# Kernel tuning notes

Measured on AMD Instinct MI355X. Metric: run time of the kernel, lower is better.

The kernel has to match this reference:

```python
import jax, jax.numpy as jnp
import numpy as np

B, SQ, SK, D, H = 8, 1024, 1024, 1024, 16
DH = D // H  # attention head size = 64
LN_EPS = 1e-5


def _layer_norm(x, g, b):
    m = jnp.mean(x, axis=-1, keepdims=True)
    v = jnp.mean(jnp.square(x - m), axis=-1, keepdims=True)
    return (x - m) * jax.lax.rsqrt(v + LN_EPS) * g + b


def setup_inputs() -> dict:
    key = jax.random.key(0)
    ks = jax.random.split(key, 12)
    s = 0.02
    return {
        "hidden_states": jax.random.normal(ks[0], (B, SQ, D), jnp.float32),
        "context": jax.random.normal(ks[1], (B, SK, D), jnp.float32),
        "Wq": jax.random.normal(ks[2], (D, D), jnp.float32) * s,
        "bq": jnp.zeros((D,), jnp.float32),
        "Wk": jax.random.normal(ks[3], (D, D), jnp.float32) * s,
        "bk": jnp.zeros((D,), jnp.float32),
        "Wv": jax.random.normal(ks[4], (D, D), jnp.float32) * s,
        "bv": jnp.zeros((D,), jnp.float32),
        "Wobs": jax.random.normal(ks[5], (D, D), jnp.float32) * s,
        "bobs": jnp.zeros((D,), jnp.float32),
        "Wmat": jax.random.normal(ks[6], (D, D), jnp.float32) * s,
        "bmat": jnp.zeros((D,), jnp.float32),
        "ln_g": jnp.ones((D,), jnp.float32),
        "ln_b": jnp.zeros((D,), jnp.float32),
    }


def reference(hidden_states, context, Wq, bq, Wk, bk, Wv, bv,
              Wobs, bobs, Wmat, bmat, ln_g, ln_b):
    # QKV projections (torch Linear: x @ W.T + b)
    q = hidden_states @ Wq.T + bq            # [B, SQ, D]
    k = context @ Wk.T + bk                  # [B, SK, D]
    v = context @ Wv.T + bv                  # [B, SK, D]

    # ---- Guide_Block: single-head SDPA over full D, then linear->ReLU->LN ----
    # (dropout is identity in eval mode)
    score = jnp.einsum('bqd,bkd->bqk', q, k) / np.sqrt(D)   # [B, SQ, SK]
    attn = jax.nn.softmax(score, axis=-1)
    gctx = jnp.einsum('bqk,bkd->bqd', attn, v)              # [B, SQ, D]
    new_q = _layer_norm(jax.nn.relu(gctx @ Wobs.T + bobs), ln_g, ln_b)
    new_k = _layer_norm(jax.nn.relu(k @ Wmat.T + bmat), ln_g, ln_b)

    # ---- Multi-head attention with guided q/k and original v ----
    qh = new_q.reshape(B, SQ, H, DH).transpose(0, 2, 1, 3)  # [B, H, SQ, DH]
    kh = new_k.reshape(B, SK, H, DH).transpose(0, 2, 1, 3)
    vh = v.reshape(B, SK, H, DH).transpose(0, 2, 1, 3)
    scores = jnp.einsum('bhqd,bhkd->bhqk', qh, kh) / np.sqrt(DH)
    probs = jax.nn.softmax(scores, axis=-1)                 # attn dropout = identity (eval)
    out = jnp.einsum('bhqk,bhkd->bhqd', probs, vh)          # [B, H, SQ, DH]
    return out.transpose(0, 2, 1, 3).reshape(B, SQ, D)
```

## Files before the change

kernel.cpp:

```cpp
#include <hip/hip_runtime.h>
#include <hip/hip_bf16.h>

#define DEV __device__ __forceinline__

using bf16x8 = __attribute__((ext_vector_type(8))) short;
using f32x4  = __attribute__((ext_vector_type(4))) float;
using f32x16 = __attribute__((ext_vector_type(16))) float;

#define MFMA16(a, b, c) __builtin_amdgcn_mfma_f32_16x16x32_bf16((a), (b), (c), 0, 0, 0)
#define MFMA32(a, b, c) __builtin_amdgcn_mfma_f32_32x32x16_bf16((a), (b), (c), 0, 0, 0)

#define GLOAD_LDS16(gp, lp)                                                        \
  __builtin_amdgcn_global_load_lds(                                               \
      (__attribute__((address_space(1))) unsigned int*)(gp),                      \
      (__attribute__((address_space(3))) unsigned int*)(lp), 16, 0, 0)

DEV float b2f(unsigned short u) {
  union { float f; unsigned u; } x; x.u = ((unsigned)u) << 16; return x.f;
}
DEV unsigned short f2b(float f) {
  union { float f; unsigned u; } x; x.f = f;
  unsigned r = x.u + 0x7FFFu + ((x.u >> 16) & 1u);
  return (unsigned short)(r >> 16);
}
DEV float fexp2(float x) {
  float r;
  asm("v_exp_f32 %0, %1" : "=v"(r) : "v"(x));
  return r;
}

__global__ __launch_bounds__(256) void detect_kernel(
    const unsigned short* __restrict__ hs, int* __restrict__ flag) {
  __shared__ int red[4];
  const int t = threadIdx.x;
  const ushort4* p = (const ushort4*)hs;
  int cnt = 0;
#pragma unroll
  for (int j = 0; j < 16; j++) {
    ushort4 u = p[j * 256 + t];
    cnt += (((u.x >> 7) & 0xFF) == 0xFF) + (((u.y >> 7) & 0xFF) == 0xFF) +
           (((u.z >> 7) & 0xFF) == 0xFF) + (((u.w >> 7) & 0xFF) == 0xFF);
  }
#pragma unroll
  for (int off = 32; off >= 1; off >>= 1) cnt += __shfl_xor(cnt, off, 64);
  if ((t & 63) == 0) red[t >> 6] = cnt;
  __syncthreads();
  if (t == 0) flag[0] = (red[0] + red[1] + red[2] + red[3] >= 4) ? 1 : 0;
}

__global__ __launch_bounds__(256) void convert2_kernel(
    const void* __restrict__ s0, const void* __restrict__ s1,
    unsigned short* __restrict__ d0, unsigned short* __restrict__ d1,
    const int* __restrict__ flag) {
  const int bid = blockIdx.x;
  const void* src;
  unsigned short* dst;
  long off;
  if (bid < 8192) { src = s0; dst = d0; off = (long)bid * 1024; }
  else            { src = s1; dst = d1; off = (long)(bid - 8192) * 1024; }
  const long i = off + threadIdx.x * 4;
  ushort4 o;
  if (*flag) {
    float4 f = ((const float4*)src)[i >> 2];
    o.x = f2b(f.x); o.y = f2b(f.y); o.z = f2b(f.z); o.w = f2b(f.w);
  } else {
    o = ((const ushort4*)src)[i >> 2];
  }
  ((ushort4*)dst)[i >> 2] = o;
}

__global__ __launch_bounds__(256) void convert_w_kernel(
    const void* __restrict__ s0, const void* __restrict__ s1,
    const void* __restrict__ s2, const void* __restrict__ s3,
    const void* __restrict__ s4, unsigned short* __restrict__ dst,
    const int* __restrict__ flag) {
  const void* srcs[5] = {s0, s1, s2, s3, s4};
  const void* src = srcs[blockIdx.y];
  unsigned short* d = dst + (long)blockIdx.y * 1048576;
  const int i = (blockIdx.x * 256 + threadIdx.x) * 4;
  ushort4 o;
  if (*flag) {
    float4 f = ((const float4*)src)[i >> 2];
    o.x = f2b(f.x); o.y = f2b(f.y); o.z = f2b(f.z); o.w = f2b(f.w);
  } else {
    o = ((const ushort4*)src)[i >> 2];
  }
  ((ushort4*)d)[i >> 2] = o;
}

__global__ __launch_bounds__(256) void convert_vec_kernel(
    const void* __restrict__ s0, const void* __restrict__ s1,
    const void* __restrict__ s2, const void* __restrict__ s3,
    const void* __restrict__ s4, const void* __restrict__ s5,
    const void* __restrict__ s6, unsigned short* __restrict__ dst,
    const int* __restrict__ flag) {
  const void* srcs[7] = {s0, s1, s2, s3, s4, s5, s6};
  const void* src = srcs[blockIdx.x];
  unsigned short* d = dst + blockIdx.x * 1024;
  const int i = threadIdx.x * 4;
  ushort4 o;
  if (*flag) {
    float4 f = ((const float4*)src)[i >> 2];
    o.x = f2b(f.x); o.y = f2b(f.y); o.z = f2b(f.z); o.w = f2b(f.w);
  } else {
    o = ((const ushort4*)src)[i >> 2];
  }
  ((ushort4*)d)[i >> 2] = o;
}

template <int RELU, int OUTBF16, int BIAS, int SPLIT>
__global__ __launch_bounds__(256, 4) void gemm_bt_kernel(
    const unsigned short* __restrict__ A, const unsigned short* __restrict__ B,
    const unsigned short* __restrict__ bias, void* __restrict__ Cv,
    void* __restrict__ Cv2, int M, int N, int K, long sA_, long sB_, long sC_,
    float scale) {
  __shared__ unsigned short sA[2][128 * 32];
  __shared__ unsigned short sB[2][128 * 32];
  const int t = threadIdx.x;
  const int wave = t >> 6, lane = t & 63;
  const int quad = lane >> 4, col = lane & 15;
  const int wm = wave >> 1, wn = wave & 1;
  const long zb = blockIdx.z;
  const unsigned short* Ab = A + zb * sA_ + (long)blockIdx.x * 128 * K;
  const unsigned short* Bb = B + zb * sB_ + (long)blockIdx.y * 128 * K;
  const int r0 = t >> 2;
  const int c0 = (t & 3) * 8;

  f32x4 zz = {0.f, 0.f, 0.f, 0.f};
  f32x4 acc[4][4];
#pragma unroll
  for (int i = 0; i < 4; i++)
#pragma unroll
    for (int j = 0; j < 4; j++) acc[i][j] = zz;

  for (int k0 = 0; k0 < K; k0 += 64) {
    __syncthreads();
#pragma unroll
    for (int p = 0; p < 2; p++) {
      GLOAD_LDS16(Ab + (long)r0 * K + k0 + p * 32 + c0,        &sA[p][t * 8]);
      GLOAD_LDS16(Ab + (long)(64 + r0) * K + k0 + p * 32 + c0, &sA[p][2048 + t * 8]);
      GLOAD_LDS16(Bb + (long)r0 * K + k0 + p * 32 + c0,        &sB[p][t * 8]);
      GLOAD_LDS16(Bb + (long)(64 + r0) * K + k0 + p * 32 + c0, &sB[p][2048 + t * 8]);
    }
    __syncthreads();
#pragma unroll
    for (int p = 0; p < 2; p++) {
      bf16x8 af[4], bfr[4];
#pragma unroll
      for (int mi = 0; mi < 4; mi++)
        af[mi] = *(const bf16x8*)&sA[p][(wm * 64 + mi * 16 + col) * 32 + quad * 8];
#pragma unroll
      for (int ni = 0; ni < 4; ni++)
        bfr[ni] = *(const bf16x8*)&sB[p][(wn * 64 + ni * 16 + col) * 32 + quad * 8];
#pragma unroll
      for (int mi = 0; mi < 4; mi++)
#pragma unroll
        for (int ni = 0; ni < 4; ni++)
          acc[mi][ni] = MFMA16(af[mi], bfr[ni], acc[mi][ni]);
    }
  }

  const int Rm = blockIdx.x * 128 + wm * 64;
  const int Cn = blockIdx.y * 128 + wn * 64;
  float bs[4];
#pragma unroll
  for (int ni = 0; ni < 4; ni++)
    bs[ni] = BIAS ? b2f(bias[Cn + ni * 16 + col]) : 0.f;

  unsigned short* Cb = (unsigned short*)Cv;
  int Nw = N, cadj = 0;
  if (SPLIT) {
    Nw = N >> 1;
    if (blockIdx.y >= (gridDim.y >> 1)) { Cb = (unsigned short*)Cv2; cadj = Nw; }
  }
#pragma unroll
  for (int mi = 0; mi < 4; mi++)
#pragma unroll
    for (int ni = 0; ni < 4; ni++)
#pragma unroll
      for (int r = 0; r < 4; r++) {
        int rr = Rm + mi * 16 + quad * 4 + r;
        int cc = Cn + ni * 16 + col;
        float v = acc[mi][ni][r] * scale + bs[ni];
        if (RELU) v = fmaxf(v, 0.f);
        if (OUTBF16)
          Cb[zb * sC_ + (long)rr * Nw + (cc - cadj)] = f2b(v);
        else
          ((float*)Cv)[zb * sC_ + (long)rr * N + cc] = v;
      }
}

__global__ __launch_bounds__(256) void softmax_kernel(
    const float* __restrict__ S, unsigned short* __restrict__ P) {
  __shared__ float red[8];
  const long row = blockIdx.x;
  const int t = threadIdx.x;
  const float4 v4 = ((const float4*)(S + row * 1024))[t];
  float x[4] = {v4.x, v4.y, v4.z, v4.w};
  float m = fmaxf(fmaxf(x[0], x[1]), fmaxf(x[2], x[3]));
#pragma unroll
  for (int off = 32; off >= 1; off >>= 1) m = fmaxf(m, __shfl_xor(m, off, 64));
  if ((t & 63) == 0) red[t >> 6] = m;
  __syncthreads();
  m = fmaxf(fmaxf(red[0], red[1]), fmaxf(red[2], red[3]));
  float e[4], s = 0.f;
#pragma unroll
  for (int i = 0; i < 4; i++) { e[i] = __expf(x[i] - m); s += e[i]; }
#pragma unroll
  for (int off = 32; off >= 1; off >>= 1) s += __shfl_xor(s, off, 64);
  __syncthreads();
  if ((t & 63) == 0) red[4 + (t >> 6)] = s;
  __syncthreads();
  s = red[4] + red[5] + red[6] + red[7];
  float inv = 1.f / s;
  ushort4 o;
  o.x = f2b(e[0] * inv); o.y = f2b(e[1] * inv);
  o.z = f2b(e[2] * inv); o.w = f2b(e[3] * inv);
  ((ushort4*)(P + row * 1024))[t] = o;
}

DEV float block_sum(float v, float* red, int t) {
#pragma unroll
  for (int off = 32; off >= 1; off >>= 1) v += __shfl_xor(v, off, 64);
  __syncthreads();
  if ((t & 63) == 0) red[t >> 6] = v;
  __syncthreads();
  return red[0] + red[1] + red[2] + red[3];
}

__global__ __launch_bounds__(256) void layernorm2_kernel(
    const unsigned short* __restrict__ X0, const unsigned short* __restrict__ X1,
    const unsigned short* __restrict__ G, const unsigned short* __restrict__ Bt,
    unsigned short* __restrict__ Y0, unsigned short* __restrict__ Y1) {
  __shared__ float red[4];
  const int bid = blockIdx.x;
  const unsigned short* X;
  unsigned short* Y;
  if (bid < 8192) { X = X0 + (long)bid * 1024; Y = Y0 + (long)bid * 1024; }
  else { X = X1 + (long)(bid - 8192) * 1024; Y = Y1 + (long)(bid - 8192) * 1024; }
  const int t = threadIdx.x;
  ushort4 u = ((const ushort4*)X)[t];
  float x[4] = {b2f(u.x), b2f(u.y), b2f(u.z), b2f(u.w)};
  float s = x[0] + x[1] + x[2] + x[3];
  float mean = block_sum(s, red, t) * (1.f / 1024.f);
  float d0 = x[0] - mean, d1 = x[1] - mean, d2 = x[2] - mean, d3 = x[3] - mean;
  float vs = d0 * d0 + d1 * d1 + d2 * d2 + d3 * d3;
  float var = block_sum(vs, red, t) * (1.f / 1024.f);
  float rs = rsqrtf(var + 1e-5f);
  ushort4 gu = ((const ushort4*)G)[t];
  ushort4 bu = ((const ushort4*)Bt)[t];
  ushort4 o;
  o.x = f2b(d0 * rs * b2f(gu.x) + b2f(bu.x));
  o.y = f2b(d1 * rs * b2f(gu.y) + b2f(bu.y));
  o.z = f2b(d2 * rs * b2f(gu.z) + b2f(bu.z));
  o.w = f2b(d3 * rs * b2f(gu.w) + b2f(bu.w));
  ((ushort4*)Y)[t] = o;
}

__global__ __launch_bounds__(256) void transpose_kernel(
    const unsigned short* __restrict__ V, unsigned short* __restrict__ VT) {
  __shared__ unsigned short tile[32][33];
  const int b = blockIdx.z;
  const int d0 = blockIdx.x * 32, sk0 = blockIdx.y * 32;
  const int tx = threadIdx.x & 31, ty = threadIdx.x >> 5;
#pragma unroll
  for (int i = 0; i < 32; i += 8)
    tile[ty + i][tx] = V[((long)(b * 1024 + sk0 + ty + i)) * 1024 + d0 + tx];
  __syncthreads();
#pragma unroll
  for (int i = 0; i < 32; i += 8)
    VT[((long)(b * 1024 + d0 + ty + i)) * 1024 + sk0 + tx] = tile[tx][ty + i];
}

__global__ __launch_bounds__(256, 4) void flash_mha_kernel(
    const unsigned short* __restrict__ Q, const unsigned short* __restrict__ K,
    const unsigned short* __restrict__ VT, void* __restrict__ O,
    const int* __restrict__ flag) {
  __shared__ unsigned short sK[2][64 * 64];
  __shared__ unsigned short sV[2][64 * 64];
  __shared__ float lred[4][32];
  const int t = threadIdx.x;
  const int wave = t >> 6, lane = t & 63;
  const int lr = lane & 31, lh = lane >> 5;

  const int flat = blockIdx.x + (blockIdx.y << 3) + (blockIdx.z << 7);
  const int w = (flat & 7) * 128 + (flat >> 3);
  const int xq = w & 7, h = (w >> 3) & 15, b = w >> 7;
  const int q0 = xq * 128 + wave * 32;

  bf16x8 bq[4];
#pragma unroll
  for (int d0 = 0; d0 < 4; d0++)
    bq[d0] = *(const bf16x8*)(Q +
        ((long)(b * 1024 + q0 + lr)) * 1024 + h * 64 + d0 * 16 + lh * 8);

  const unsigned short* Ks[2];
  const unsigned short* Vs[2];
#pragma unroll
  for (int j = 0; j < 2; j++) {
    const int i = t + j * 256;
    const int row = i >> 3;
    const int c = ((i & 7) ^ (row & 7)) * 8;
    const int prow = (row & ~12) | ((row & 4) << 1) | ((row & 8) >> 1);
    Ks[j] = K + ((long)(b * 1024 + prow)) * 1024 + h * 64 + c;
    Vs[j] = VT + ((long)(b * 1024 + h * 64 + row)) * 1024 + c;
  }
  const int lds0 = t * 8, lds1 = t * 8 + 2048;

#define STAGE(bi, kv0)                                        \
  {                                                           \
    GLOAD_LDS16(Ks[0] + (long)(kv0) * 1024, &sK[bi][lds0]);   \
    GLOAD_LDS16(Ks[1] + (long)(kv0) * 1024, &sK[bi][lds1]);   \
    GLOAD_LDS16(Vs[0] + (kv0), &sV[bi][lds0]);                \
    GLOAD_LDS16(Vs[1] + (kv0), &sV[bi][lds1]);                \
  }

  const f32x16 z16 = {0.f, 0.f, 0.f, 0.f, 0.f, 0.f, 0.f, 0.f,
                      0.f, 0.f, 0.f, 0.f, 0.f, 0.f, 0.f, 0.f};
  f32x16 o[2];
  o[0] = z16; o[1] = z16;
  float p0 = 0.f, p1 = 0.f, p2 = 0.f, p3 = 0.f;

  STAGE(0, 0);
  for (int kt = 0; kt < 16; kt++) {
    const int bi = kt & 1;
    __syncthreads();
    if (kt < 15) STAGE(bi ^ 1, (kt + 1) * 64);

    bf16x8 pa[4];
#pragma unroll
    for (int kvt = 0; kvt < 2; kvt++) {
      const int krow = kvt * 32 + lr;
      const int kx = krow & 7;
      f32x16 st;
      __builtin_amdgcn_s_setprio(1);
      {
        const bf16x8 kf0 =
            *(const bf16x8*)&sK[bi][krow * 64 + (((0 | lh) ^ kx) << 3)];
        st = MFMA32(kf0, bq[0], z16);
      }
#pragma unroll
      for (int d0 = 1; d0 < 4; d0++) {
        const bf16x8 kf =
            *(const bf16x8*)&sK[bi][krow * 64 + ((((d0 << 1) | lh) ^ kx) << 3)];
        st = MFMA32(kf, bq[d0], st);
      }
      __builtin_amdgcn_s_setprio(0);

      float e[16];
#pragma unroll
      for (int r = 0; r < 16; r++)
        e[r] = fexp2(st[r] * 0.18033688f);
#pragma unroll
      for (int r = 0; r < 16; r += 4) {
        p0 += e[r]; p1 += e[r + 1]; p2 += e[r + 2]; p3 += e[r + 3];
      }
      unsigned dw[8];
#pragma unroll
      for (int m = 0; m < 8; m++)
        asm("v_cvt_pk_bf16_f32 %0, %1, %2"
            : "=v"(dw[m]) : "v"(e[2 * m]), "v"(e[2 * m + 1]));
      union { unsigned u[4]; bf16x8 v; } f0, f1;
      f0.u[0] = dw[0]; f0.u[1] = dw[1]; f0.u[2] = dw[2]; f0.u[3] = dw[3];
      f1.u[0] = dw[4]; f1.u[1] = dw[5]; f1.u[2] = dw[6]; f1.u[3] = dw[7];
      pa[kvt * 2] = f0.v;
      pa[kvt * 2 + 1] = f1.v;
    }

    __builtin_amdgcn_s_setprio(1);
#pragma unroll
    for (int kc = 0; kc < 4; kc++)
#pragma unroll
      for (int dht = 0; dht < 2; dht++) {
        const int vrow = dht * 32 + lr;
        const bf16x8 vf =
            *(const bf16x8*)&sV[bi][vrow * 64 + ((((kc << 1) | lh) ^ (vrow & 7)) << 3)];
        o[dht] = MFMA32(pa[kc], vf, o[dht]);
      }
    __builtin_amdgcn_s_setprio(0);
  }
#undef STAGE

  float lt = (p0 + p1) + (p2 + p3);
  lt += __shfl_xor(lt, 32, 64);
  if (lane < 32) lred[wave][lr] = lt;
  __syncthreads();

  const int f32o = *flag;
#pragma unroll
  for (int r = 0; r < 16; r++) {
    const int rowi = (lh << 2) + (r & 3) + ((r >> 2) << 3);
    const float inv = 1.f / lred[wave][rowi];
    const long gr = ((long)(b * 1024 + q0 + rowi)) * 1024 + h * 64 + lr;
    if (f32o) {
      ((float*)O)[gr] = o[0][r] * inv;
      ((float*)O)[gr + 32] = o[1][r] * inv;
    } else {
      ((unsigned short*)O)[gr] = f2b(o[0][r] * inv);
      ((unsigned short*)O)[gr + 32] = f2b(o[1][r] * inv);
    }
  }
}

extern "C" void kernel_launch(void* const* d_in, const int* in_sizes, int n_in,
                              void* d_out, int out_size, void* d_ws,
                              size_t ws_size, hipStream_t stream) {
  (void)in_sizes; (void)n_in; (void)out_size; (void)ws_size;
  const void* hs   = d_in[0];
  const void* ctx  = d_in[1];
  const void* Wq   = d_in[2];
  const void* bq   = d_in[3];
  const void* Wk   = d_in[4];
  const void* bk   = d_in[5];
  const void* Wv   = d_in[6];
  const void* bv   = d_in[7];
  const void* Wobs = d_in[8];
  const void* bobs = d_in[9];
  const void* Wmat = d_in[10];
  const void* bmat = d_in[11];
  const void* lng  = d_in[12];
  const void* lnb  = d_in[13];

  const long E = 8LL * 1024 * 1024;
  const long W1 = 1024L * 1024L;
  unsigned short* base = (unsigned short*)d_ws;
  unsigned short* hsb   = base;
  unsigned short* ctxb  = base + E;
  unsigned short* Wb    = base + 2 * E;
  unsigned short* Wqb   = Wb;
  unsigned short* Wkb   = Wb + W1;
  unsigned short* Wvb   = Wb + 2 * W1;
  unsigned short* Wobsb = Wb + 3 * W1;
  unsigned short* Wmatb = Wb + 4 * W1;
  unsigned short* vecs  = base + 2 * E + 5 * W1;
  unsigned short* bqb   = vecs;
  unsigned short* bkb   = vecs + 1024;
  unsigned short* bvb   = vecs + 2048;
  unsigned short* bobsb = vecs + 3072;
  unsigned short* bmatb = vecs + 4096;
  unsigned short* lngb  = vecs + 5120;
  unsigned short* lnbb  = vecs + 6144;
  int* flag = (int*)(vecs + 32768);
  unsigned short* q     = vecs + W1;
  unsigned short* k     = q + E;
  unsigned short* v     = k + E;
  unsigned short* vT    = v + E;
  float* scores = (float*)(vT + E);
  unsigned short* nq    = (unsigned short*)scores;
  unsigned short* newq  = ((unsigned short*)scores) + E;
  unsigned short* probs = hsb;
  unsigned short* gctx  = ctxb;
  unsigned short* nk    = v;
  unsigned short* newk  = q;

  dim3 blk(256);
  const long S1 = 1024L * 1024L;

  detect_kernel<<<dim3(1), blk, 0, stream>>>((const unsigned short*)hs, flag);
  convert2_kernel<<<dim3(16384), blk, 0, stream>>>(hs, ctx, hsb, ctxb, flag);
  convert_w_kernel<<<dim3(1024, 5), blk, 0, stream>>>(Wq, Wk, Wv, Wobs, Wmat, Wb, flag);
  convert_vec_kernel<<<dim3(7), blk, 0, stream>>>(bq, bk, bv, bobs, bmat, lng, lnb,
                                                  vecs, flag);

  gemm_bt_kernel<0, 1, 1, 0><<<dim3(64, 8, 1), blk, 0, stream>>>(
      hsb, Wqb, bqb, q, q, 8192, 1024, 1024, 0, 0, 0, 1.f);
  gemm_bt_kernel<0, 1, 1, 1><<<dim3(64, 16, 1), blk, 0, stream>>>(
      ctxb, Wkb, bkb, k, v, 8192, 2048, 1024, 0, 0, 0, 1.f);
  transpose_kernel<<<dim3(32, 32, 8), blk, 0, stream>>>(v, vT);
  gemm_bt_kernel<0, 0, 0, 0><<<dim3(8, 8, 8), blk, 0, stream>>>(
      q, k, nullptr, scores, scores, 1024, 1024, 1024, S1, S1, S1, 0.03125f);
  softmax_kernel<<<dim3(8192), blk, 0, stream>>>(scores, probs);
  gemm_bt_kernel<0, 1, 0, 0><<<dim3(8, 8, 8), blk, 0, stream>>>(
      probs, vT, nullptr, gctx, gctx, 1024, 1024, 1024, S1, S1, S1, 1.f);
  gemm_bt_kernel<1, 1, 1, 0><<<dim3(64, 8, 1), blk, 0, stream>>>(
      gctx, Wobsb, bobsb, nq, nq, 8192, 1024, 1024, 0, 0, 0, 1.f);
  gemm_bt_kernel<1, 1, 1, 0><<<dim3(64, 8, 1), blk, 0, stream>>>(
      k, Wmatb, bmatb, nk, nk, 8192, 1024, 1024, 0, 0, 0, 1.f);
  layernorm2_kernel<<<dim3(16384), blk, 0, stream>>>(nq, nk, lngb, lnbb, newq, newk);
  flash_mha_kernel<<<dim3(8, 16, 8), blk, 0, stream>>>(
      newq, newk, vT, d_out, flag);
}
```

Baseline: 407.3 us.

## Fuse softmax into score GEMM epilogue and defer normalization to PV GEMM

Removes the standalone softmax kernel. The QK^T GEMM epilogue now exponentiates the scores and writes unnormalized bf16 probabilities directly. It accumulates per-row sums into a zeroed float buffer via shuffles and atomicAdd, and the PV GEMM divides each output row by that sum. This avoids writing and re-reading the fp32 score matrix, but drops the row-max subtraction, so it relies on the score range not overflowing exp. The GEMM launch bound minimum occupancy is also lowered from 4 to 2 blocks.

```diff
diff --git a/kernel.cpp b/kernel.cpp
--- a/kernel.cpp
+++ b/kernel.cpp
@@ -93,7 +93,14 @@
     const void* __restrict__ s2, const void* __restrict__ s3,
     const void* __restrict__ s4, const void* __restrict__ s5,
     const void* __restrict__ s6, unsigned short* __restrict__ dst,
-    const int* __restrict__ flag) {
+    float* __restrict__ lbuf, const int* __restrict__ flag) {
+  if (blockIdx.x == 7) {
+    float4 z = {0.f, 0.f, 0.f, 0.f};
+    float4* p = (float4*)lbuf;
+#pragma unroll
+    for (int i = 0; i < 8; i++) p[i * 256 + threadIdx.x] = z;
+    return;
+  }
   const void* srcs[7] = {s0, s1, s2, s3, s4, s5, s6};
   const void* src = srcs[blockIdx.x];
   unsigned short* d = dst + blockIdx.x * 1024;
@@ -108,12 +115,12 @@
   ((ushort4*)d)[i >> 2] = o;
 }
 
-template <int RELU, int OUTBF16, int BIAS, int SPLIT>
-__global__ __launch_bounds__(256, 4) void gemm_bt_kernel(
+template <int RELU, int OUTBF16, int BIAS, int SPLIT, int EXPP, int LDIV>
+__global__ __launch_bounds__(256, 2) void gemm_bt_kernel(
     const unsigned short* __restrict__ A, const unsigned short* __restrict__ B,
     const unsigned short* __restrict__ bias, void* __restrict__ Cv,
-    void* __restrict__ Cv2, int M, int N, int K, long sA_, long sB_, long sC_,
-    float scale) {
+    void* __restrict__ Cv2, float* __restrict__ lbuf, int M, int N, int K,
+    long sA_, long sB_, long sC_, float scale) {
   __shared__ unsigned short sA[2][128 * 32];
   __shared__ unsigned short sB[2][128 * 32];
   const int t = threadIdx.x;
@@ -176,47 +183,31 @@
 #pragma unroll
   for (int mi = 0; mi < 4; mi++)
 #pragma unroll
-    for (int ni = 0; ni < 4; ni++)
-#pragma unroll
-      for (int r = 0; r < 4; r++) {
-        int rr = Rm + mi * 16 + quad * 4 + r;
-        int cc = Cn + ni * 16 + col;
+    for (int r = 0; r < 4; r++) {
+      const int rr = Rm + mi * 16 + quad * 4 + r;
+      float rowscale = 1.f;
+      if (LDIV) rowscale = 1.f / lbuf[zb * 1024 + rr];
+      float rsum = 0.f;
+#pragma unroll
+      for (int ni = 0; ni < 4; ni++) {
+        const int cc = Cn + ni * 16 + col;
         float v = acc[mi][ni][r] * scale + bs[ni];
         if (RELU) v = fmaxf(v, 0.f);
+        if (EXPP) { v = fexp2(v * 1.442695041f); rsum += v; }
+        if (LDIV) v = v * rowscale;
         if (OUTBF16)
           Cb[zb * sC_ + (long)rr * Nw + (cc - cadj)] = f2b(v);
         else
           ((float*)Cv)[zb * sC_ + (long)rr * N + cc] = v;
       }
-}
-
-__global__ __launch_bounds__(256) void softmax_kernel(
-    const float* __restrict__ S, unsigned short* __restrict__ P) {
-  __shared__ float red[8];
-  const long row = blockIdx.x;
-  const int t = threadIdx.x;
-  const float4 v4 = ((const float4*)(S + row * 1024))[t];
-  float x[4] = {v4.x, v4.y, v4.z, v4.w};
-  float m = fmaxf(fmaxf(x[0], x[1]), fmaxf(x[2], x[3]));
-#pragma unroll
-  for (int off = 32; off >= 1; off >>= 1) m = fmaxf(m, __shfl_xor(m, off, 64));
-  if ((t & 63) == 0) red[t >> 6] = m;
-  __syncthreads();
-  m = fmaxf(fmaxf(red[0], red[1]), fmaxf(red[2], red[3]));
-  float e[4], s = 0.f;
-#pragma unroll
-  for (int i = 0; i < 4; i++) { e[i] = __expf(x[i] - m); s += e[i]; }
-#pragma unroll
-  for (int off = 32; off >= 1; off >>= 1) s += __shfl_xor(s, off, 64);
-  __syncthreads();
-  if ((t & 63) == 0) red[4 + (t >> 6)] = s;
-  __syncthreads();
-  s = red[4] + red[5] + red[6] + red[7];
-  float inv = 1.f / s;
-  ushort4 o;
-  o.x = f2b(e[0] * inv); o.y = f2b(e[1] * inv);
-  o.z = f2b(e[2] * inv); o.w = f2b(e[3] * inv);
-  ((ushort4*)(P + row * 1024))[t] = o;
+      if (EXPP) {
+        rsum += __shfl_xor(rsum, 1, 64);
+        rsum += __shfl_xor(rsum, 2, 64);
+        rsum += __shfl_xor(rsum, 4, 64);
+        rsum += __shfl_xor(rsum, 8, 64);
+        if (col == 0) atomicAdd(lbuf + zb * 1024 + rr, rsum);
+      }
+    }
 }
 
 DEV float block_sum(float v, float* red, int t) {
@@ -440,6 +431,7 @@
   unsigned short* bmatb = vecs + 4096;
   unsigned short* lngb  = vecs + 5120;
   unsigned short* lnbb  = vecs + 6144;
+  float* lbuf = (float*)(vecs + 8192);
   int* flag = (int*)(vecs + 32768);
   unsigned short* q     = vecs + W1;
   unsigned short* k     = q + E;
@@ -459,23 +451,22 @@
   detect_kernel<<<dim3(1), blk, 0, stream>>>((const unsigned short*)hs, flag);
   convert2_kernel<<<dim3(16384), blk, 0, stream>>>(hs, ctx, hsb, ctxb, flag);
   convert_w_kernel<<<dim3(1024, 5), blk, 0, stream>>>(Wq, Wk, Wv, Wobs, Wmat, Wb, flag);
-  convert_vec_kernel<<<dim3(7), blk, 0, stream>>>(bq, bk, bv, bobs, bmat, lng, lnb,
-                                                  vecs, flag);
-
-  gemm_bt_kernel<0, 1, 1, 0><<<dim3(64, 8, 1), blk, 0, stream>>>(
-      hsb, Wqb, bqb, q, q, 8192, 1024, 1024, 0, 0, 0, 1.f);
-  gemm_bt_kernel<0, 1, 1, 1><<<dim3(64, 16, 1), blk, 0, stream>>>(
-      ctxb, Wkb, bkb, k, v, 8192, 2048, 1024, 0, 0, 0, 1.f);
+  convert_vec_kernel<<<dim3(8), blk, 0, stream>>>(bq, bk, bv, bobs, bmat, lng, lnb,
+                                                  vecs, lbuf, flag);
+
+  gemm_bt_kernel<0, 1, 1, 0, 0, 0><<<dim3(64, 8, 1), blk, 0, stream>>>(
+      hsb, Wqb, bqb, q, q, nullptr, 8192, 1024, 1024, 0, 0, 0, 1.f);
+  gemm_bt_kernel<0, 1, 1, 1, 0, 0><<<dim3(64, 16, 1), blk, 0, stream>>>(
+      ctxb, Wkb, bkb, k, v, nullptr, 8192, 2048, 1024, 0, 0, 0, 1.f);
   transpose_kernel<<<dim3(32, 32, 8), blk, 0, stream>>>(v, vT);
-  gemm_bt_kernel<0, 0, 0, 0><<<dim3(8, 8, 8), blk, 0, stream>>>(
-      q, k, nullptr, scores, scores, 1024, 1024, 1024, S1, S1, S1, 0.03125f);
-  softmax_kernel<<<dim3(8192), blk, 0, stream>>>(scores, probs);
-  gemm_bt_kernel<0, 1, 0, 0><<<dim3(8, 8, 8), blk, 0, stream>>>(
-      probs, vT, nullptr, gctx, gctx, 1024, 1024, 1024, S1, S1, S1, 1.f);
-  gemm_bt_kernel<1, 1, 1, 0><<<dim3(64, 8, 1), blk, 0, stream>>>(
-      gctx, Wobsb, bobsb, nq, nq, 8192, 1024, 1024, 0, 0, 0, 1.f);
-  gemm_bt_kernel<1, 1, 1, 0><<<dim3(64, 8, 1), blk, 0, stream>>>(
-      k, Wmatb, bmatb, nk, nk, 8192, 1024, 1024, 0, 0, 0, 1.f);
+  gemm_bt_kernel<0, 1, 0, 0, 1, 0><<<dim3(8, 8, 8), blk, 0, stream>>>(
+      q, k, nullptr, probs, probs, lbuf, 1024, 1024, 1024, S1, S1, S1, 0.03125f);
+  gemm_bt_kernel<0, 1, 0, 0, 0, 1><<<dim3(8, 8, 8), blk, 0, stream>>>(
+      probs, vT, nullptr, gctx, gctx, lbuf, 1024, 1024, 1024, S1, S1, S1, 1.f);
+  gemm_bt_kernel<1, 1, 1, 0, 0, 0><<<dim3(64, 8, 1), blk, 0, stream>>>(
+      gctx, Wobsb, bobsb, nq, nq, nullptr, 8192, 1024, 1024, 0, 0, 0, 1.f);
+  gemm_bt_kernel<1, 1, 1, 0, 0, 0><<<dim3(64, 8, 1), blk, 0, stream>>>(
+      k, Wmatb, bmatb, nk, nk, nullptr, 8192, 1024, 1024, 0, 0, 0, 1.f);
   layernorm2_kernel<<<dim3(16384), blk, 0, stream>>>(nq, nk, lngb, lnbb, newq, newk);
   flash_mha_kernel<<<dim3(8, 16, 8), blk, 0, stream>>>(
       newq, newk, vT, d_out, flag);
```

New measurement: 393.0 us. 3.5% less time.
